# Kernel optimization log

Measured on AMD Instinct MI355X. Metric: run time of the kernel, lower is better.

Reference implementation:

```python
import jax, jax.numpy as jnp
import numpy as np

HEADS = 16
DIM_HEAD = 64
DIM = 1024
INNER = HEADS * DIM_HEAD  # 1024
SCALE = DIM_HEAD ** -0.5
SCALE_ = INNER ** -0.5
B, NM1 = 8, 1023  # mask is [b, n-1]; n = 1024 after CLS pad


def setup_inputs() -> dict:
    key = jax.random.key(0)
    k_x, k_m, k_w1, k_w2, k_b = jax.random.split(key, 5)
    x = jax.random.normal(k_x, (B, NM1 + 1, DIM), dtype=jnp.float32)
    mask = jax.random.randint(k_m, (B, NM1), 0, 2).astype(jnp.bool_)
    # torch Linear(dim, 3*inner, bias=False): y = x @ W.T; store as [dim, 3*inner]
    w_qkv = jax.random.normal(k_w1, (DIM, 3 * INNER), dtype=jnp.float32) * (DIM ** -0.5)
    w_out = jax.random.normal(k_w2, (INNER, DIM), dtype=jnp.float32) * (INNER ** -0.5)
    b_out = jax.random.normal(k_b, (DIM,), dtype=jnp.float32) * 0.01
    return {"x": x, "mask": mask, "w_qkv": w_qkv, "w_out": w_out, "b_out": b_out}


def reference(x, mask, w_qkv, w_out, b_out):
    b, n, _ = x.shape
    qkv = x @ w_qkv                                   # [b, n, 3*inner]
    q_, k_, v_ = jnp.split(qkv, 3, axis=-1)           # each [b, n, inner]

    # pooled-token attention on un-headed Q, K
    attn_ = jax.nn.softmax(jnp.einsum('bik,bjk->bij', q_, k_) * SCALE_, axis=-1)

    # multi-head attention
    def to_heads(t):
        return t.reshape(b, n, HEADS, DIM_HEAD).transpose(0, 2, 1, 3)  # [b, h, n, d]
    q, k, v = to_heads(q_), to_heads(k_), to_heads(v_)
    dots = jnp.einsum('bhid,bhjd->bhij', q, k) * SCALE  # [b, h, n, n]

    mask_value = -jnp.finfo(dots.dtype).max
    m = jnp.pad(mask, ((0, 0), (1, 0)), constant_values=True)  # prepend CLS=True -> [b, n]
    full = m[:, None, None, :] & m[:, None, :, None]           # [b, 1, n, n]
    dots = jnp.where(full, dots, mask_value)

    attn = jax.nn.softmax(dots, axis=-1)
    out = jnp.einsum('bhij,bhjd->bhid', attn, v)       # [b, h, n, d]
    out = out.transpose(0, 2, 1, 3).reshape(b, n, INNER)
    out = out @ w_out + b_out                          # dropout is identity (p=0, eval)
    return out, attn_
```

## Files before the change

### kernel.cpp

```cpp
#include <hip/hip_runtime.h>

typedef _Float16 f16;
typedef _Float16 f16x8 __attribute__((ext_vector_type(8)));
typedef _Float16 f16x4 __attribute__((ext_vector_type(4)));
typedef float    f32x4 __attribute__((ext_vector_type(4)));

#define DEV __device__ __forceinline__

DEV void gload16(const void* g, void* l) {
  __builtin_amdgcn_global_load_lds(
      (const __attribute__((address_space(1))) unsigned int*)g,
      (__attribute__((address_space(3))) unsigned int*)l, 16, 0, 0);
}

__global__ void cast_f16(const float* __restrict__ s, f16* __restrict__ d, int n4) {
  int i = blockIdx.x * blockDim.x + threadIdx.x;
  if (i < n4) {
    float4 v = ((const float4*)s)[i];
    f16x4 o;
    o[0] = (f16)v.x; o[1] = (f16)v.y; o[2] = (f16)v.z; o[3] = (f16)v.w;
    ((f16x4*)d)[i] = o;
  }
}

__global__ void transpose_cast(const float* __restrict__ src, f16* __restrict__ dst,
                               int R, int C) {
  __shared__ float tile[64][65];
  const int cb = blockIdx.x * 64, rb = blockIdx.y * 64;
  const int tx = threadIdx.x & 63, ty = threadIdx.x >> 6;
#pragma unroll
  for (int i = 0; i < 64; i += 4)
    tile[ty + i][tx] = src[(size_t)(rb + ty + i) * C + cb + tx];
  __syncthreads();
#pragma unroll
  for (int i = 0; i < 64; i += 4)
    dst[(size_t)(cb + ty + i) * R + rb + tx] = (f16)tile[tx][ty + i];
}

__global__ void prep_mask(const void* __restrict__ mask, unsigned char* __restrict__ mpad) {
  int i = blockIdx.x * blockDim.x + threadIdx.x;
  if (i >= 8192) return;
  const unsigned int* wv = (const unsigned int*)mask;
  bool anyf32 = false, anybig = false;
  for (int k = 0; k < 64; k++) {
    unsigned int x = wv[k];
    if (x == 0x3f800000u) anyf32 = true;
    else if (x > 1u) anybig = true;
  }
  int b = i >> 10, j = i & 1023;
  bool v;
  if (j == 0) v = true;
  else {
    size_t idx = (size_t)b * 1023 + (j - 1);
    if (anyf32)      v = ((const float*)mask)[idx] != 0.f;
    else if (anybig) v = ((const unsigned char*)mask)[idx] != 0;
    else             v = ((const int*)mask)[idx] != 0;
  }
  mpad[i] = v ? 1 : 0;
}

template <int MODE>
__global__ __launch_bounds__(256, 2) void gemm_nt(
    const f16* __restrict__ A, int lda, long sAb,
    const f16* __restrict__ Bt, int ldb, long sBb,
    float* __restrict__ Cf, long sCb,
    const float* __restrict__ bias,
    f16* __restrict__ qkb, f16* __restrict__ vTb,
    int N, int K) {
  __shared__ __align__(16) f16 As[128 * 32];
  __shared__ __align__(16) f16 Bs[128 * 32];
  const int tid = threadIdx.x;
  const int w = tid >> 6, l = tid & 63;
  const int lr = l & 15, lg = l >> 4;
  const int wm = w >> 1, wn = w & 1;
  const int m0 = blockIdx.y * 128, n0 = blockIdx.x * 128;
  const int z = blockIdx.z;
  const f16* Ab = A + (size_t)z * sAb;
  const f16* Btb = Bt + (size_t)z * sBb;

  const f32x4 zero4 = {0.f, 0.f, 0.f, 0.f};
  f32x4 acc[4][4];
#pragma unroll
  for (int m = 0; m < 4; m++)
#pragma unroll
    for (int n = 0; n < 4; n++) acc[m][n] = zero4;

  const int srow = l >> 2;
  const int sch = (l & 3) ^ (srow & 3);

  for (int k0 = 0; k0 < K; k0 += 32) {
#pragma unroll
    for (int i = 0; i < 2; i++) {
      int blk = w * 2 + i;
      int row = blk * 16 + srow;
      gload16(Ab + (size_t)(m0 + row) * lda + k0 + sch * 8, (void*)(As + blk * 512));
      gload16(Btb + (size_t)(n0 + row) * ldb + k0 + sch * 8, (void*)(Bs + blk * 512));
    }
    __syncthreads();
    f16x8 af[4], bf[4];
#pragma unroll
    for (int m = 0; m < 4; m++) {
      int row = wm * 64 + m * 16 + lr;
      af[m] = *(const f16x8*)&As[row * 32 + ((lg ^ (row & 3)) << 3)];
    }
#pragma unroll
    for (int n = 0; n < 4; n++) {
      int row = wn * 64 + n * 16 + lr;
      bf[n] = *(const f16x8*)&Bs[row * 32 + ((lg ^ (row & 3)) << 3)];
    }
#pragma unroll
    for (int m = 0; m < 4; m++)
#pragma unroll
      for (int n = 0; n < 4; n++)
        acc[m][n] = __builtin_amdgcn_mfma_f32_16x16x32_f16(af[m], bf[n], acc[m][n], 0, 0, 0);
    __syncthreads();
  }

#pragma unroll
  for (int m = 0; m < 4; m++) {
    const int rb0 = m0 + wm * 64 + m * 16 + lg * 4;
#pragma unroll
    for (int n = 0; n < 4; n++) {
      const int c = n0 + wn * 64 + n * 16 + lr;
      if constexpr (MODE == 0) {
        if (c < 2048) {
#pragma unroll
          for (int ri = 0; ri < 4; ri++) {
            int rr = rb0 + ri;
            qkb[(size_t)(rr >> 10) * 2097152 + (size_t)(rr & 1023) * 2048 + c] =
                (f16)acc[m][n][ri];
          }
        } else {
          int bb = rb0 >> 10, nn = rb0 & 1023;
          f16x4 pk;
#pragma unroll
          for (int ri = 0; ri < 4; ri++) pk[ri] = (f16)acc[m][n][ri];
          *(f16x4*)(vTb + (size_t)bb * 1048576 + (size_t)(c - 2048) * 1024 + nn) = pk;
        }
      } else if constexpr (MODE == 1) {
        float* Cz = Cf + (size_t)z * sCb;
#pragma unroll
        for (int ri = 0; ri < 4; ri++)
          Cz[(size_t)(rb0 + ri) * N + c] = acc[m][n][ri] * 0.03125f;
      } else {
        float bv = bias[c];
#pragma unroll
        for (int ri = 0; ri < 4; ri++)
          Cf[(size_t)(rb0 + ri) * N + c] = acc[m][n][ri] + bv;
      }
    }
  }
}

__global__ __launch_bounds__(256) void softmax_rows(float* __restrict__ p) {
  __shared__ float redm[4], reds[4];
  float* row = p + (size_t)blockIdx.x * 1024;
  const int t = threadIdx.x;
  float4 v = ((const float4*)row)[t];
  float mx = fmaxf(fmaxf(v.x, v.y), fmaxf(v.z, v.w));
#pragma unroll
  for (int d = 1; d < 64; d <<= 1) mx = fmaxf(mx, __shfl_xor(mx, d));
  if ((t & 63) == 0) redm[t >> 6] = mx;
  __syncthreads();
  mx = fmaxf(fmaxf(redm[0], redm[1]), fmaxf(redm[2], redm[3]));
  v.x = __expf(v.x - mx); v.y = __expf(v.y - mx);
  v.z = __expf(v.z - mx); v.w = __expf(v.w - mx);
  float s = v.x + v.y + v.z + v.w;
#pragma unroll
  for (int d = 1; d < 64; d <<= 1) s += __shfl_xor(s, d);
  if ((t & 63) == 0) reds[t >> 6] = s;
  __syncthreads();
  s = reds[0] + reds[1] + reds[2] + reds[3];
  float inv = 1.0f / s;
  v.x *= inv; v.y *= inv; v.z *= inv; v.w *= inv;
  ((float4*)row)[t] = v;
}

__global__ __launch_bounds__(256, 2) void flash_kernel(
    const f16* __restrict__ qkb,
    const f16* __restrict__ vTb,
    const unsigned char* __restrict__ mpad,
    f16* __restrict__ ob) {
  __shared__ __align__(16) f16 Ks[2][64 * 64];
  __shared__ __align__(16) f16 Vts[2][64 * 64];
  __shared__ __align__(16) f16 Ps[4][64 * 64];

  const int tid = threadIdx.x;
  const int w = tid >> 6, l = tid & 63;
  const int lr = l & 15, lg = l >> 4;
  const int bh = blockIdx.x, qt = blockIdx.y;
  const int h = bh & 15, b = bh >> 4;
  const int qbase = qt * 256 + w * 64;
  const f16* qk_b = qkb + (size_t)b * 2097152;
  const f16* vT_b = vTb + (size_t)b * 1048576 + (size_t)h * 64 * 1024;
  const unsigned char* mp = mpad + b * 1024;

  const int srow = l >> 3;
  const int schunk = (l & 7) ^ srow;

  auto stage = [&](int buf, int t) {
#pragma unroll
    for (int i = 0; i < 2; i++) {
      int blk = w * 2 + i;
      int row = blk * 8 + srow;
      gload16(qk_b + 1024 + (size_t)(t * 64 + row) * 2048 + h * 64 + schunk * 8,
              (void*)(Ks[buf] + blk * 512));
      gload16(vT_b + (size_t)row * 1024 + t * 64 + schunk * 8,
              (void*)(Vts[buf] + blk * 512));
    }
  };

  stage(0, 0);

  f16x8 qf[4][2];
#pragma unroll
  for (int m = 0; m < 4; m++)
#pragma unroll
    for (int kk = 0; kk < 2; kk++) {
      int row = qbase + m * 16 + lr;
      int col = h * 64 + kk * 32 + lg * 8;
      qf[m][kk] = *(const f16x8*)(qk_b + (size_t)row * 2048 + col);
    }

  unsigned int mi4 = 0;
#pragma unroll
  for (int m = 0; m < 4; m++)
    mi4 |= (mp[qbase + m * 16 + lr] ? 1u : 0u) << m;

  const f32x4 zero4 = {0.f, 0.f, 0.f, 0.f};
  float mrun[4], lrun[4];
  f32x4 oacc[4][4];
#pragma unroll
  for (int m = 0; m < 4; m++) {
    mrun[m] = -3e38f; lrun[m] = 0.f;
#pragma unroll
    for (int i = 0; i < 4; i++) oacc[m][i] = zero4;
  }

  __syncthreads();

  for (int t = 0; t < 16; t++) {
    const int cur = t & 1;
    if (t < 15) stage(cur ^ 1, t + 1);

    f32x4 st[4][4];
#pragma unroll
    for (int n = 0; n < 4; n++)
#pragma unroll
      for (int m = 0; m < 4; m++) st[n][m] = zero4;
#pragma unroll
    for (int kk = 0; kk < 2; kk++)
#pragma unroll
      for (int n = 0; n < 4; n++) {
        int krow = n * 16 + lr;
        int ch = (kk * 4 + lg) ^ (krow & 7);
        f16x8 kf = *(const f16x8*)&Ks[cur][krow * 64 + ch * 8];
#pragma unroll
        for (int m = 0; m < 4; m++)
          st[n][m] = __builtin_amdgcn_mfma_f32_16x16x32_f16(kf, qf[m][kk], st[n][m], 0, 0, 0);
      }

    unsigned int mw[4];
#pragma unroll
    for (int n = 0; n < 4; n++)
      mw[n] = *(const unsigned int*)(mp + t * 64 + n * 16 + lg * 4);

#pragma unroll
    for (int m = 0; m < 4; m++) {
      const bool rowok = (mi4 >> m) & 1;
      float sv[4][4];
      float vmax = -3e38f;
#pragma unroll
      for (int n = 0; n < 4; n++)
#pragma unroll
        for (int ri = 0; ri < 4; ri++) {
          float s = st[n][m][ri];
          bool ok = ((mw[n] >> (8 * ri)) & 255u) != 0u;
          s = rowok ? (ok ? s * 0.125f : -1e30f) : 0.f;
          sv[n][ri] = s;
          vmax = fmaxf(vmax, s);
        }
      vmax = fmaxf(vmax, __shfl_xor(vmax, 16));
      vmax = fmaxf(vmax, __shfl_xor(vmax, 32));
      float nm_ = fmaxf(mrun[m], vmax);
      float sc = __expf(mrun[m] - nm_);
      mrun[m] = nm_;
      float rs = 0.f;
      const int qr = m * 16 + lr;
#pragma unroll
      for (int n = 0; n < 4; n++) {
        f16x4 pk;
#pragma unroll
        for (int ri = 0; ri < 4; ri++) {
          float pp = __expf(sv[n][ri] - nm_);
          rs += pp;
          pk[ri] = (f16)pp;
        }
        const int col0 = n * 16 + lg * 4;
        const int swz = (col0 >> 3) ^ (qr & 7);
        *(f16x4*)&Ps[w][qr * 64 + swz * 8 + (col0 & 7)] = pk;
      }
      rs += __shfl_xor(rs, 16);
      rs += __shfl_xor(rs, 32);
      lrun[m] = lrun[m] * sc + rs;
      float scb[4];
#pragma unroll
      for (int ri = 0; ri < 4; ri++) scb[ri] = __shfl(sc, lg * 4 + ri);
#pragma unroll
      for (int dn = 0; dn < 4; dn++)
#pragma unroll
        for (int ri = 0; ri < 4; ri++) oacc[m][dn][ri] *= scb[ri];
    }
    asm volatile("s_waitcnt lgkmcnt(0)" ::: "memory");
    __builtin_amdgcn_sched_barrier(0);

#pragma unroll
    for (int kk = 0; kk < 2; kk++) {
      f16x8 pa[4];
#pragma unroll
      for (int m = 0; m < 4; m++) {
        int qr = m * 16 + lr;
        int ch = (kk * 4 + lg) ^ (qr & 7);
        pa[m] = *(const f16x8*)&Ps[w][qr * 64 + ch * 8];
      }
#pragma unroll
      for (int dn = 0; dn < 4; dn++) {
        int vrow = dn * 16 + lr;
        int ch = (kk * 4 + lg) ^ (vrow & 7);
        f16x8 vf = *(const f16x8*)&Vts[cur][vrow * 64 + ch * 8];
#pragma unroll
        for (int m = 0; m < 4; m++)
          oacc[m][dn] = __builtin_amdgcn_mfma_f32_16x16x32_f16(pa[m], vf, oacc[m][dn], 0, 0, 0);
      }
    }
    __syncthreads();
  }

#pragma unroll
  for (int m = 0; m < 4; m++) {
    float lb[4];
#pragma unroll
    for (int ri = 0; ri < 4; ri++) lb[ri] = __shfl(lrun[m], lg * 4 + ri);
#pragma unroll
    for (int dn = 0; dn < 4; dn++)
#pragma unroll
      for (int ri = 0; ri < 4; ri++) {
        int qg = qbase + m * 16 + lg * 4 + ri;
        float o = oacc[m][dn][ri] / lb[ri];
        ob[(size_t)(b * 1024 + qg) * 1024 + h * 64 + dn * 16 + lr] = (f16)o;
      }
  }
}

extern "C" void kernel_launch(void* const* d_in, const int* in_sizes, int n_in,
                              void* d_out, int out_size, void* d_ws, size_t ws_size,
                              hipStream_t stream) {
  const float* x     = (const float*)d_in[0];
  const void*  mask  = d_in[1];
  const float* w_qkv = (const float*)d_in[2];
  const float* w_out = (const float*)d_in[3];
  const float* b_out = (const float*)d_in[4];
  float* out  = (float*)d_out;
  float* attn = out + 8388608;

  char* ws = (char*)d_ws;
  f16* xb    = (f16*)(ws);
  f16* wqkvT = (f16*)(ws + 16777216);
  f16* woutT = (f16*)(ws + 23068672);
  f16* qkb   = (f16*)(ws + 25165824);
  f16* vTb   = (f16*)(ws + 58720256);
  f16* ob    = xb;
  unsigned char* mpad = (unsigned char*)(ws + 75497472);

  cast_f16<<<8192, 256, 0, stream>>>(x, xb, 2097152);
  transpose_cast<<<dim3(48, 16), 256, 0, stream>>>(w_qkv, wqkvT, 1024, 3072);
  transpose_cast<<<dim3(16, 16), 256, 0, stream>>>(w_out, woutT, 1024, 1024);
  prep_mask<<<32, 256, 0, stream>>>(mask, mpad);

  gemm_nt<0><<<dim3(24, 64), 256, 0, stream>>>(xb, 1024, 0, wqkvT, 1024, 0,
                                               nullptr, 0, nullptr, qkb, vTb, 3072, 1024);
  gemm_nt<1><<<dim3(8, 8, 8), 256, 0, stream>>>(qkb, 2048, 2097152, qkb + 1024, 2048, 2097152,
                                                attn, 1048576, nullptr, nullptr, nullptr, 1024, 1024);
  softmax_rows<<<8192, 256, 0, stream>>>(attn);

  flash_kernel<<<dim3(128, 4), 256, 0, stream>>>(qkb, vTb, mpad, ob);

  gemm_nt<2><<<dim3(8, 64), 256, 0, stream>>>(ob, 1024, 0, woutT, 1024, 0,
                                              out, 0, b_out, nullptr, nullptr, 1024, 1024);
}
```

Baseline: 338.2 us.

## Rewrite GEMM as 8-wave 256x128 tile with double-buffered LDS pipeline

Replaces the 4-wave 128x128, K=32 single-buffered GEMM with an 8-wave kernel computing 256x128 tiles at K=64 per step. Global-to-LDS loads for the next K tile are issued in two halves, interleaved with two MFMA phases that use explicit waitcnt, s_barrier and setprio. The goal is to hide load latency and raise MFMA utilization for the QKV, pooled-attention and output projections. In exchange it uses about 96KB of LDS for one block per CU, hardcodes K=1024 (16 iterations), and depends on a barrier/waitcnt choreography that is easy to get subtly wrong.

Result: faster. 301.6 us (-10.8%).

```diff
diff --git a/kernel.cpp b/kernel.cpp
--- a/kernel.cpp
+++ b/kernel.cpp
@@ -60,24 +60,37 @@
 }
 
 template <int MODE>
-__global__ __launch_bounds__(256, 2) void gemm_nt(
+__global__ __launch_bounds__(512, 1) void gemm8(
     const f16* __restrict__ A, int lda, long sAb,
     const f16* __restrict__ Bt, int ldb, long sBb,
     float* __restrict__ Cf, long sCb,
     const float* __restrict__ bias,
-    f16* __restrict__ qkb, f16* __restrict__ vTb,
-    int N, int K) {
-  __shared__ __align__(16) f16 As[128 * 32];
-  __shared__ __align__(16) f16 Bs[128 * 32];
+    f16* __restrict__ qkb, f16* __restrict__ vTb, int N) {
+  __shared__ __align__(16) f16 smem[2 * 24576];
   const int tid = threadIdx.x;
   const int w = tid >> 6, l = tid & 63;
   const int lr = l & 15, lg = l >> 4;
   const int wm = w >> 1, wn = w & 1;
-  const int m0 = blockIdx.y * 128, n0 = blockIdx.x * 128;
+  const int m0 = blockIdx.y * 256, n0 = blockIdx.x * 128;
   const int z = blockIdx.z;
   const f16* Ab = A + (size_t)z * sAb;
   const f16* Btb = Bt + (size_t)z * sBb;
 
+  const int gr = w * 8 + (l >> 3);
+  const int gsch = (l & 7) ^ (l >> 3);
+
+  auto stageA = [&](int buf, int kt, int r) {
+    gload16(Ab + (size_t)(m0 + r * 64 + gr) * lda + kt * 64 + gsch * 8,
+            (void*)(smem + buf * 24576 + r * 4096 + w * 512));
+  };
+  auto stageB = [&](int buf, int kt, int r) {
+    gload16(Btb + (size_t)(n0 + r * 64 + gr) * ldb + kt * 64 + gsch * 8,
+            (void*)(smem + buf * 24576 + 16384 + r * 4096 + w * 512));
+  };
+
+  stageA(0, 0, 0); stageA(0, 0, 1); stageA(0, 0, 2); stageA(0, 0, 3);
+  stageB(0, 0, 0); stageB(0, 0, 1);
+
   const f32x4 zero4 = {0.f, 0.f, 0.f, 0.f};
   f32x4 acc[4][4];
 #pragma unroll
@@ -85,35 +98,73 @@
 #pragma unroll
     for (int n = 0; n < 4; n++) acc[m][n] = zero4;
 
-  const int srow = l >> 2;
-  const int sch = (l & 3) ^ (srow & 3);
-
-  for (int k0 = 0; k0 < K; k0 += 32) {
-#pragma unroll
-    for (int i = 0; i < 2; i++) {
-      int blk = w * 2 + i;
-      int row = blk * 16 + srow;
-      gload16(Ab + (size_t)(m0 + row) * lda + k0 + sch * 8, (void*)(As + blk * 512));
-      gload16(Btb + (size_t)(n0 + row) * ldb + k0 + sch * 8, (void*)(Bs + blk * 512));
-    }
-    __syncthreads();
-    f16x8 af[4], bf[4];
-#pragma unroll
-    for (int m = 0; m < 4; m++) {
-      int row = wm * 64 + m * 16 + lr;
-      af[m] = *(const f16x8*)&As[row * 32 + ((lg ^ (row & 3)) << 3)];
-    }
-#pragma unroll
-    for (int n = 0; n < 4; n++) {
-      int row = wn * 64 + n * 16 + lr;
-      bf[n] = *(const f16x8*)&Bs[row * 32 + ((lg ^ (row & 3)) << 3)];
-    }
-#pragma unroll
-    for (int m = 0; m < 4; m++)
+  for (int T = 0; T < 16; ++T) {
+    const int cur = T & 1, nxt = cur ^ 1;
+    const f16* pA = smem + cur * 24576;
+    const f16* pB = pA + 16384;
+
+    if (T < 15) {
+      stageA(nxt, T + 1, 0); stageA(nxt, T + 1, 1); stageA(nxt, T + 1, 2);
+      asm volatile("s_waitcnt vmcnt(3)" ::: "memory");
+    } else {
+      asm volatile("s_waitcnt vmcnt(0)" ::: "memory");
+    }
+    __builtin_amdgcn_s_barrier();
+
+    f16x8 bf[4][2], af[2][2];
+#pragma unroll
+    for (int n = 0; n < 4; n++)
+#pragma unroll
+      for (int kk = 0; kk < 2; kk++) {
+        int row = wn * 64 + n * 16 + lr;
+        bf[n][kk] = *(const f16x8*)&pB[row * 64 + (((kk * 4 + lg) ^ (row & 7)) << 3)];
+      }
+#pragma unroll
+    for (int mi = 0; mi < 2; mi++)
+#pragma unroll
+      for (int kk = 0; kk < 2; kk++) {
+        int row = wm * 64 + mi * 16 + lr;
+        af[mi][kk] = *(const f16x8*)&pA[row * 64 + (((kk * 4 + lg) ^ (row & 7)) << 3)];
+      }
+    asm volatile("s_waitcnt lgkmcnt(0)" ::: "memory");
+    __builtin_amdgcn_sched_barrier(0);
+    __builtin_amdgcn_s_setprio(1);
+#pragma unroll
+    for (int mi = 0; mi < 2; mi++)
 #pragma unroll
       for (int n = 0; n < 4; n++)
-        acc[m][n] = __builtin_amdgcn_mfma_f32_16x16x32_f16(af[m], bf[n], acc[m][n], 0, 0, 0);
-    __syncthreads();
+#pragma unroll
+        for (int kk = 0; kk < 2; kk++)
+          acc[mi][n] = __builtin_amdgcn_mfma_f32_16x16x32_f16(af[mi][kk], bf[n][kk], acc[mi][n], 0, 0, 0);
+    __builtin_amdgcn_s_setprio(0);
+    __builtin_amdgcn_sched_barrier(0);
+    __builtin_amdgcn_s_barrier();
+
+    f16x8 af2[2][2];
+#pragma unroll
+    for (int mi = 0; mi < 2; mi++)
+#pragma unroll
+      for (int kk = 0; kk < 2; kk++) {
+        int row = wm * 64 + (2 + mi) * 16 + lr;
+        af2[mi][kk] = *(const f16x8*)&pA[row * 64 + (((kk * 4 + lg) ^ (row & 7)) << 3)];
+      }
+    if (T < 15) {
+      stageA(nxt, T + 1, 3); stageB(nxt, T + 1, 0); stageB(nxt, T + 1, 1);
+    }
+    __builtin_amdgcn_s_barrier();
+    asm volatile("s_waitcnt lgkmcnt(0)" ::: "memory");
+    __builtin_amdgcn_sched_barrier(0);
+    __builtin_amdgcn_s_setprio(1);
+#pragma unroll
+    for (int mi = 0; mi < 2; mi++)
+#pragma unroll
+      for (int n = 0; n < 4; n++)
+#pragma unroll
+        for (int kk = 0; kk < 2; kk++)
+          acc[2 + mi][n] = __builtin_amdgcn_mfma_f32_16x16x32_f16(af2[mi][kk], bf[n][kk], acc[2 + mi][n], 0, 0, 0);
+    __builtin_amdgcn_s_setprio(0);
+    __builtin_amdgcn_sched_barrier(0);
+    __builtin_amdgcn_s_barrier();
   }
 
 #pragma unroll
@@ -377,14 +428,14 @@
   transpose_cast<<<dim3(16, 16), 256, 0, stream>>>(w_out, woutT, 1024, 1024);
   prep_mask<<<32, 256, 0, stream>>>(mask, mpad);
 
-  gemm_nt<0><<<dim3(24, 64), 256, 0, stream>>>(xb, 1024, 0, wqkvT, 1024, 0,
-                                               nullptr, 0, nullptr, qkb, vTb, 3072, 1024);
-  gemm_nt<1><<<dim3(8, 8, 8), 256, 0, stream>>>(qkb, 2048, 2097152, qkb + 1024, 2048, 2097152,
-                                                attn, 1048576, nullptr, nullptr, nullptr, 1024, 1024);
+  gemm8<0><<<dim3(24, 32), 512, 0, stream>>>(xb, 1024, 0, wqkvT, 1024, 0,
+                                             nullptr, 0, nullptr, qkb, vTb, 3072);
+  gemm8<1><<<dim3(8, 4, 8), 512, 0, stream>>>(qkb, 2048, 2097152, qkb + 1024, 2048, 2097152,
+                                              attn, 1048576, nullptr, nullptr, nullptr, 1024);
   softmax_rows<<<8192, 256, 0, stream>>>(attn);
 
   flash_kernel<<<dim3(128, 4), 256, 0, stream>>>(qkb, vTb, mpad, ob);
 
-  gemm_nt<2><<<dim3(8, 64), 256, 0, stream>>>(ob, 1024, 0, woutT, 1024, 0,
-                                              out, 0, b_out, nullptr, nullptr, 1024, 1024);
-}
+  gemm8<2><<<dim3(8, 32), 512, 0, stream>>>(ob, 1024, 0, woutT, 1024, 0,
+                                            out, 0, b_out, nullptr, nullptr, 1024);
+}
```
